# Kernel optimization log

Measured on AMD Instinct MI355X. Metric: run time of the kernel, lower is better.

Reference implementation:

```python
import jax, jax.numpy as jnp
import numpy as np

Q, N, FDIM, HDIM = 4096, 1024, 64, 128


def setup_inputs() -> dict:
    key = jax.random.key(0)
    ks = jax.random.split(key, 7)
    s = 0.05
    return {
        "query_points": jax.random.normal(ks[0], (Q, 3), dtype=jnp.float32),
        "node_features": jax.random.normal(ks[1], (N, FDIM), dtype=jnp.float32),
        "node_positions": jax.random.normal(ks[2], (N, 3), dtype=jnp.float32),
        # attention MLP: Linear(F+3 -> H), ReLU, Linear(H -> 1)
        "aW1": jax.random.normal(ks[3], (FDIM + 3, HDIM), dtype=jnp.float32) * s,
        "ab1": jnp.zeros((HDIM,), dtype=jnp.float32),
        "aW2": jax.random.normal(ks[4], (HDIM, 1), dtype=jnp.float32) * s,
        "ab2": jnp.zeros((1,), dtype=jnp.float32),
        # decoder MLP: Linear(F -> H), ReLU, Linear(H -> 3)
        "dW1": jax.random.normal(ks[5], (FDIM, HDIM), dtype=jnp.float32) * s,
        "db1": jnp.zeros((HDIM,), dtype=jnp.float32),
        "dW2": jax.random.normal(ks[6], (HDIM, 3), dtype=jnp.float32) * s,
        "db2": jnp.zeros((3,), dtype=jnp.float32),
    }


def reference(query_points, node_features, node_positions,
              aW1, ab1, aW2, ab2, dW1, db1, dW2, db2):
    F = node_features.shape[1]
    # pairwise offsets: [Q, N, 3]
    diff = query_points[:, None, :] - node_positions[None, :, :]
    # xy-plane distance -> inverse-distance weights: [Q, N, 1]
    dist = jnp.linalg.norm(diff[..., :2], axis=-1, keepdims=True)
    w = 1.0 / (dist + 1e-6)
    # attn MLP on concat([node_features, diff]); split W1 so the feature
    # part ([N,F]@[F,H]) is computed once instead of per query pair.
    h = jax.nn.relu(node_features @ aW1[:F] + diff @ aW1[F:] + ab1)  # [Q, N, H]
    score = h @ aW2 + ab2                                            # [Q, N, 1]
    attn = jax.nn.softmax(score * w, axis=1)                         # [Q, N, 1]
    agg = jnp.einsum('qn,nf->qf', attn[..., 0], node_features)       # [Q, F]
    return jax.nn.relu(agg @ dW1 + db1) @ dW2 + db2                  # [Q, 3]
```

## Files before the change

kernel.cpp:

```cpp
#include <hip/hip_runtime.h>
#include <math.h>

#define QN 4096
#define NN 1024
#define FD 64
#define HD 128

#define OFF_UT    0
#define OFF_B     524288
#define OFF_L     655360
#define OFF_PM    4849664
#define OFF_PART  4980736
#define OFF_SPART 7077888

__global__ __launch_bounds__(256) void k1_prep(
    const float* __restrict__ qp, const float* __restrict__ nf,
    const float* __restrict__ npos, const float* __restrict__ aW1,
    const float* __restrict__ ab1, float* __restrict__ B, float* __restrict__ UT) {
  int idx = blockIdx.x * 256 + threadIdx.x;
  if (idx < QN * HD) {
    int h = idx >> 12, q = idx & 4095;
    UT[idx] = qp[q*3+0] * aW1[(FD+0)*HD + h]
            + qp[q*3+1] * aW1[(FD+1)*HD + h]
            + qp[q*3+2] * aW1[(FD+2)*HD + h];
  } else {
    int i2 = idx - QN * HD;
    if (i2 < NN * HD) {
      int n = i2 >> 7, h = i2 & 127;
      float s = ab1[h];
      #pragma unroll
      for (int f = 0; f < FD; ++f) s = fmaf(nf[n*FD+f], aW1[f*HD+h], s);
      s -= npos[n*3+0] * aW1[(FD+0)*HD + h]
         + npos[n*3+1] * aW1[(FD+1)*HD + h]
         + npos[n*3+2] * aW1[(FD+2)*HD + h];
      B[i2] = s;
    }
  }
}

__global__ __launch_bounds__(256) void k2_logits(
    const float* __restrict__ Bg, const float* __restrict__ UT,
    const float* __restrict__ aW2, const float* __restrict__ ab2,
    const float* __restrict__ qp, const float* __restrict__ npos,
    float* __restrict__ L, float* __restrict__ pm) {
  __shared__ float Bs[32 * HD];
  __shared__ float red[4][4][64];
  const int q0 = blockIdx.x * 256, n0 = blockIdx.y * 32;
  const int t = threadIdx.x;
  {
    const float4* src = (const float4*)(Bg + n0 * HD);
    float4* dst = (float4*)Bs;
    #pragma unroll
    for (int r = 0; r < 4; ++r) dst[r*256 + t] = src[r*256 + t];
  }
  __syncthreads();
  const int lane = t & 63, w = t >> 6;
  const int nb = w * 8;

  float acc[4][8];
  #pragma unroll
  for (int qq = 0; qq < 4; ++qq)
    #pragma unroll
    for (int nn = 0; nn < 8; ++nn) acc[qq][nn] = 0.f;

  for (int hc = 0; hc < 16; ++hc) {
    float u[4][8];
    #pragma unroll
    for (int hh = 0; hh < 8; ++hh) {
      const float* up = UT + (hc*8 + hh) * QN + q0 + lane;
      #pragma unroll
      for (int qq = 0; qq < 4; ++qq) u[qq][hh] = up[qq*64];
    }
    float v[8];
    #pragma unroll
    for (int hh = 0; hh < 8; ++hh) v[hh] = aW2[hc*8 + hh];

    #pragma unroll
    for (int nn = 0; nn < 8; ++nn) {
      const float4* bp = (const float4*)(Bs + (nb + nn) * HD + hc*8);
      float4 b0 = bp[0], b1 = bp[1];
      float bb[8] = {b0.x, b0.y, b0.z, b0.w, b1.x, b1.y, b1.z, b1.w};
      #pragma unroll
      for (int qq = 0; qq < 4; ++qq) {
        #pragma unroll
        for (int hh = 0; hh < 8; ++hh) {
          float r = fmaxf(bb[hh] + u[qq][hh], 0.f);
          acc[qq][nn] = fmaf(r, v[hh], acc[qq][nn]);
        }
      }
    }
  }

  const float bias2 = ab2[0];
  float qx[4], qy[4], m4[4];
  #pragma unroll
  for (int qq = 0; qq < 4; ++qq) {
    int q = q0 + qq*64 + lane;
    qx[qq] = qp[q*3+0];
    qy[qq] = qp[q*3+1];
    m4[qq] = -3.4e38f;
  }
  #pragma unroll
  for (int nn = 0; nn < 8; ++nn) {
    int n = n0 + nb + nn;
    float px = npos[n*3+0], py = npos[n*3+1];
    #pragma unroll
    for (int qq = 0; qq < 4; ++qq) {
      float dx = qx[qq] - px, dy = qy[qq] - py;
      float wgt = 1.f / (sqrtf(dx*dx + dy*dy) + 1e-6f);
      float lg = (acc[qq][nn] + bias2) * wgt;
      L[n * QN + q0 + qq*64 + lane] = lg;
      m4[qq] = fmaxf(m4[qq], lg);
    }
  }
  #pragma unroll
  for (int qq = 0; qq < 4; ++qq) red[w][qq][lane] = m4[qq];
  __syncthreads();
  {
    int qq = t >> 6, ll = t & 63;
    float mm = fmaxf(fmaxf(red[0][qq][ll], red[1][qq][ll]),
                     fmaxf(red[2][qq][ll], red[3][qq][ll]));
    pm[(q0 + qq*64 + ll) * 32 + blockIdx.y] = mm;
  }
}

__global__ __launch_bounds__(256) void k4_agg(
    const float* __restrict__ L, const float* __restrict__ pm,
    const float* __restrict__ nf, float* __restrict__ part,
    float* __restrict__ spart) {
  __shared__ float red[4][32][64];
  __shared__ float sred[4][64];
  int b = blockIdx.x;
  int qt = b & 63, c = b >> 6;
  int t = threadIdx.x, lane = t & 63, w = t >> 6;
  int q = qt * 64 + lane;

  float m = -3.4e38f;
  {
    const float4* pmq = (const float4*)(pm + q * 32);
    #pragma unroll
    for (int g = 0; g < 8; ++g) {
      float4 pv = pmq[g];
      m = fmaxf(m, fmaxf(fmaxf(pv.x, pv.y), fmaxf(pv.z, pv.w)));
    }
  }

  float acc[64];
  #pragma unroll
  for (int f = 0; f < 64; ++f) acc[f] = 0.f;
  float s = 0.f;

  int nbase = c * 128 + w * 32;
  for (int i = 0; i < 32; ++i) {
    int n = nbase + i;
    float p = exp2f((L[n * QN + q] - m) * 1.44269504088896f);
    s += p;
    const float4* nfr = (const float4*)(nf + n * FD);
    #pragma unroll
    for (int g = 0; g < 4; ++g) {
      float4 a0 = nfr[g*4+0], a1 = nfr[g*4+1], a2 = nfr[g*4+2], a3 = nfr[g*4+3];
      acc[g*16+ 0] = fmaf(p, a0.x, acc[g*16+ 0]);
      acc[g*16+ 1] = fmaf(p, a0.y, acc[g*16+ 1]);
      acc[g*16+ 2] = fmaf(p, a0.z, acc[g*16+ 2]);
      acc[g*16+ 3] = fmaf(p, a0.w, acc[g*16+ 3]);
      acc[g*16+ 4] = fmaf(p, a1.x, acc[g*16+ 4]);
      acc[g*16+ 5] = fmaf(p, a1.y, acc[g*16+ 5]);
      acc[g*16+ 6] = fmaf(p, a1.z, acc[g*16+ 6]);
      acc[g*16+ 7] = fmaf(p, a1.w, acc[g*16+ 7]);
      acc[g*16+ 8] = fmaf(p, a2.x, acc[g*16+ 8]);
      acc[g*16+ 9] = fmaf(p, a2.y, acc[g*16+ 9]);
      acc[g*16+10] = fmaf(p, a2.z, acc[g*16+10]);
      acc[g*16+11] = fmaf(p, a2.w, acc[g*16+11]);
      acc[g*16+12] = fmaf(p, a3.x, acc[g*16+12]);
      acc[g*16+13] = fmaf(p, a3.y, acc[g*16+13]);
      acc[g*16+14] = fmaf(p, a3.z, acc[g*16+14]);
      acc[g*16+15] = fmaf(p, a3.w, acc[g*16+15]);
    }
  }

  sred[w][lane] = s;
  #pragma unroll
  for (int f = 0; f < 32; ++f) red[w][f][lane] = acc[f];
  __syncthreads();
  for (int idx = t; idx < 2048; idx += 256) {
    int f = idx >> 6, qq = idx & 63;
    float sum = red[0][f][qq] + red[1][f][qq] + red[2][f][qq] + red[3][f][qq];
    part[(c*64 + f) * QN + qt*64 + qq] = sum;
  }
  __syncthreads();
  #pragma unroll
  for (int f = 0; f < 32; ++f) red[w][f][lane] = acc[32 + f];
  __syncthreads();
  for (int idx = t; idx < 2048; idx += 256) {
    int f = idx >> 6, qq = idx & 63;
    float sum = red[0][f][qq] + red[1][f][qq] + red[2][f][qq] + red[3][f][qq];
    part[(c*64 + 32 + f) * QN + qt*64 + qq] = sum;
  }
  __syncthreads();
  if (t < 64) {
    spart[c * QN + qt*64 + t] = sred[0][t] + sred[1][t] + sred[2][t] + sred[3][t];
  }
}

__global__ __launch_bounds__(256) void k5_dec(
    const float* __restrict__ part, const float* __restrict__ spart,
    const float* __restrict__ dW1, const float* __restrict__ db1,
    const float* __restrict__ dW2, const float* __restrict__ db2,
    float* __restrict__ out) {
  __shared__ float aggL[2][64];
  __shared__ float h1s[2][128];
  int t = threadIdx.x;
  int qb = blockIdx.x * 2;
  if (t < 128) {
    int q2 = t >> 6, f = t & 63;
    int q = qb + q2;
    float v = 0.f;
    #pragma unroll
    for (int c = 0; c < 8; ++c) v += part[(c*64 + f) * QN + q];
    float s = 0.f;
    #pragma unroll
    for (int c = 0; c < 8; ++c) s += spart[c * QN + q];
    aggL[q2][f] = v / s;
  }
  __syncthreads();
  {
    int q2 = t >> 7, h = t & 127;
    float a = db1[h];
    #pragma unroll
    for (int f = 0; f < 64; ++f) a = fmaf(aggL[q2][f], dW1[f*HD + h], a);
    h1s[q2][h] = fmaxf(a, 0.f);
  }
  __syncthreads();
  if (t < 6) {
    int q2 = t / 3, o = t % 3;
    float a = db2[o];
    #pragma unroll
    for (int h = 0; h < 128; ++h) a = fmaf(h1s[q2][h], dW2[h*3 + o], a);
    out[(qb + q2) * 3 + o] = a;
  }
}

extern "C" void kernel_launch(void* const* d_in, const int* in_sizes, int n_in,
                              void* d_out, int out_size, void* d_ws, size_t ws_size,
                              hipStream_t stream) {
  const float* qp   = (const float*)d_in[0];
  const float* nf   = (const float*)d_in[1];
  const float* npos = (const float*)d_in[2];
  const float* aW1  = (const float*)d_in[3];
  const float* ab1  = (const float*)d_in[4];
  const float* aW2  = (const float*)d_in[5];
  const float* ab2  = (const float*)d_in[6];
  const float* dW1  = (const float*)d_in[7];
  const float* db1  = (const float*)d_in[8];
  const float* dW2  = (const float*)d_in[9];
  const float* db2  = (const float*)d_in[10];

  float* ws    = (float*)d_ws;
  float* UT    = ws + OFF_UT;
  float* B     = ws + OFF_B;
  float* L     = ws + OFF_L;
  float* pm    = ws + OFF_PM;
  float* part  = ws + OFF_PART;
  float* spart = ws + OFF_SPART;

  hipLaunchKernelGGL(k1_prep, dim3(2560), dim3(256), 0, stream,
                     qp, nf, npos, aW1, ab1, B, UT);
  hipLaunchKernelGGL(k2_logits, dim3(16, 32), dim3(256), 0, stream,
                     B, UT, aW2, ab2, qp, npos, L, pm);
  hipLaunchKernelGGL(k4_agg, dim3(512), dim3(256), 0, stream, L, pm, nf, part, spart);
  hipLaunchKernelGGL(k5_dec, dim3(2048), dim3(256), 0, stream,
                     part, spart, dW1, db1, dW2, db2, (float*)d_out);
}
```

Measured before the change: 121.9 us.

## Halve logits node tile, double-buffer U loads, transpose partials, batch decoder queries

The logits kernel now gives each block 16 nodes instead of 32, doubling the grid. It also loads the U tiles in a software-pipelined double buffer with an occupancy hint in launch bounds. The partial-aggregate layout becomes query-major so the decoder can read it coalesced, with the LDS reduction buffer padded. The decoder handles 16 queries per block and folds the softmax normalisation after the first matmul. The aim is better occupancy and latency hiding in the dominant kernel and fewer, more efficient decoder blocks, at the cost of more redundant U reads across node tiles.

```diff
diff --git a/kernel.cpp b/kernel.cpp
--- a/kernel.cpp
+++ b/kernel.cpp
@@ -10,8 +10,8 @@
 #define OFF_B     524288
 #define OFF_L     655360
 #define OFF_PM    4849664
-#define OFF_PART  4980736
-#define OFF_SPART 7077888
+#define OFF_PART  5111808
+#define OFF_SPART 7208960
 
 __global__ __launch_bounds__(256) void k1_prep(
     const float* __restrict__ qp, const float* __restrict__ nf,
@@ -38,58 +38,63 @@
   }
 }
 
-__global__ __launch_bounds__(256) void k2_logits(
+
+#define LOADU(dst, hcv) { \
+  const float* up_ = uptr + (hcv)*8*QN; \
+  _Pragma("unroll") for (int hh = 0; hh < 8; ++hh) \
+    _Pragma("unroll") for (int qq = 0; qq < 4; ++qq) \
+      dst[qq][hh] = up_[hh*QN + qq*64]; }
+
+#define COMPUTE(u, hcv) { \
+  float vv[8]; \
+  _Pragma("unroll") for (int hh = 0; hh < 8; ++hh) vv[hh] = aW2[(hcv)*8 + hh]; \
+  _Pragma("unroll") for (int nn = 0; nn < 4; ++nn) { \
+    const float4* bp = (const float4*)(Bs + (nb + nn) * HD + (hcv)*8); \
+    float4 b0 = bp[0], b1 = bp[1]; \
+    float bb[8] = {b0.x,b0.y,b0.z,b0.w,b1.x,b1.y,b1.z,b1.w}; \
+    _Pragma("unroll") for (int qq = 0; qq < 4; ++qq) \
+      _Pragma("unroll") for (int hh = 0; hh < 8; ++hh) { \
+        float r = fmaxf(bb[hh] + u[qq][hh], 0.f); \
+        acc[qq][nn] = fmaf(r, vv[hh], acc[qq][nn]); } } }
+
+__global__ __launch_bounds__(256, 4) void k2_logits(
     const float* __restrict__ Bg, const float* __restrict__ UT,
     const float* __restrict__ aW2, const float* __restrict__ ab2,
     const float* __restrict__ qp, const float* __restrict__ npos,
     float* __restrict__ L, float* __restrict__ pm) {
-  __shared__ float Bs[32 * HD];
+  __shared__ float Bs[16 * HD];
   __shared__ float red[4][4][64];
-  const int q0 = blockIdx.x * 256, n0 = blockIdx.y * 32;
+  const int q0 = blockIdx.x * 256, n0 = blockIdx.y * 16;
   const int t = threadIdx.x;
   {
     const float4* src = (const float4*)(Bg + n0 * HD);
     float4* dst = (float4*)Bs;
     #pragma unroll
-    for (int r = 0; r < 4; ++r) dst[r*256 + t] = src[r*256 + t];
+    for (int r = 0; r < 2; ++r) dst[r*256 + t] = src[r*256 + t];
   }
   __syncthreads();
   const int lane = t & 63, w = t >> 6;
-  const int nb = w * 8;
-
-  float acc[4][8];
+  const int nb = w * 4;
+  const float* uptr = UT + q0 + lane;
+
+  float acc[4][4];
   #pragma unroll
   for (int qq = 0; qq < 4; ++qq)
     #pragma unroll
-    for (int nn = 0; nn < 8; ++nn) acc[qq][nn] = 0.f;
-
-  for (int hc = 0; hc < 16; ++hc) {
-    float u[4][8];
-    #pragma unroll
-    for (int hh = 0; hh < 8; ++hh) {
-      const float* up = UT + (hc*8 + hh) * QN + q0 + lane;
-      #pragma unroll
-      for (int qq = 0; qq < 4; ++qq) u[qq][hh] = up[qq*64];
-    }
-    float v[8];
-    #pragma unroll
-    for (int hh = 0; hh < 8; ++hh) v[hh] = aW2[hc*8 + hh];
-
-    #pragma unroll
-    for (int nn = 0; nn < 8; ++nn) {
-      const float4* bp = (const float4*)(Bs + (nb + nn) * HD + hc*8);
-      float4 b0 = bp[0], b1 = bp[1];
-      float bb[8] = {b0.x, b0.y, b0.z, b0.w, b1.x, b1.y, b1.z, b1.w};
-      #pragma unroll
-      for (int qq = 0; qq < 4; ++qq) {
-        #pragma unroll
-        for (int hh = 0; hh < 8; ++hh) {
-          float r = fmaxf(bb[hh] + u[qq][hh], 0.f);
-          acc[qq][nn] = fmaf(r, v[hh], acc[qq][nn]);
-        }
-      }
-    }
-  }
+    for (int nn = 0; nn < 4; ++nn) acc[qq][nn] = 0.f;
+
+  float uA[4][8], uB[4][8];
+  LOADU(uA, 0);
+  #pragma unroll 1
+  for (int hc = 0; hc < 14; hc += 2) {
+    LOADU(uB, hc + 1);
+    COMPUTE(uA, hc);
+    LOADU(uA, hc + 2);
+    COMPUTE(uB, hc + 1);
+  }
+  LOADU(uB, 15);
+  COMPUTE(uA, 14);
+  COMPUTE(uB, 15);
 
   const float bias2 = ab2[0];
   float qx[4], qy[4], m4[4];
@@ -101,7 +106,7 @@
     m4[qq] = -3.4e38f;
   }
   #pragma unroll
-  for (int nn = 0; nn < 8; ++nn) {
+  for (int nn = 0; nn < 4; ++nn) {
     int n = n0 + nb + nn;
     float px = npos[n*3+0], py = npos[n*3+1];
     #pragma unroll
@@ -120,7 +125,7 @@
     int qq = t >> 6, ll = t & 63;
     float mm = fmaxf(fmaxf(red[0][qq][ll], red[1][qq][ll]),
                      fmaxf(red[2][qq][ll], red[3][qq][ll]));
-    pm[(q0 + qq*64 + ll) * 32 + blockIdx.y] = mm;
+    pm[(q0 + qq*64 + ll) * 64 + blockIdx.y] = mm;
   }
 }
 
@@ -128,7 +133,7 @@
     const float* __restrict__ L, const float* __restrict__ pm,
     const float* __restrict__ nf, float* __restrict__ part,
     float* __restrict__ spart) {
-  __shared__ float red[4][32][64];
+  __shared__ float red[4][32][65];
   __shared__ float sred[4][64];
   int b = blockIdx.x;
   int qt = b & 63, c = b >> 6;
@@ -137,9 +142,9 @@
 
   float m = -3.4e38f;
   {
-    const float4* pmq = (const float4*)(pm + q * 32);
-    #pragma unroll
-    for (int g = 0; g < 8; ++g) {
+    const float4* pmq = (const float4*)(pm + q * 64);
+    #pragma unroll
+    for (int g = 0; g < 16; ++g) {
       float4 pv = pmq[g];
       m = fmaxf(m, fmaxf(fmaxf(pv.x, pv.y), fmaxf(pv.z, pv.w)));
     }
@@ -183,18 +188,18 @@
   for (int f = 0; f < 32; ++f) red[w][f][lane] = acc[f];
   __syncthreads();
   for (int idx = t; idx < 2048; idx += 256) {
-    int f = idx >> 6, qq = idx & 63;
-    float sum = red[0][f][qq] + red[1][f][qq] + red[2][f][qq] + red[3][f][qq];
-    part[(c*64 + f) * QN + qt*64 + qq] = sum;
+    int qq = idx >> 5, fr = idx & 31;
+    float sum = red[0][fr][qq] + red[1][fr][qq] + red[2][fr][qq] + red[3][fr][qq];
+    part[(c * QN + qt*64 + qq) * 64 + fr] = sum;
   }
   __syncthreads();
   #pragma unroll
   for (int f = 0; f < 32; ++f) red[w][f][lane] = acc[32 + f];
   __syncthreads();
   for (int idx = t; idx < 2048; idx += 256) {
-    int f = idx >> 6, qq = idx & 63;
-    float sum = red[0][f][qq] + red[1][f][qq] + red[2][f][qq] + red[3][f][qq];
-    part[(c*64 + 32 + f) * QN + qt*64 + qq] = sum;
+    int qq = idx >> 5, fr = idx & 31;
+    float sum = red[0][fr][qq] + red[1][fr][qq] + red[2][fr][qq] + red[3][fr][qq];
+    part[(c * QN + qt*64 + qq) * 64 + 32 + fr] = sum;
   }
   __syncthreads();
   if (t < 64) {
@@ -207,36 +212,47 @@
     const float* __restrict__ dW1, const float* __restrict__ db1,
     const float* __restrict__ dW2, const float* __restrict__ db2,
     float* __restrict__ out) {
-  __shared__ float aggL[2][64];
-  __shared__ float h1s[2][128];
+  __shared__ float agg[16][64];
+  __shared__ float inv[16];
+  __shared__ float h1s[16][128];
   int t = threadIdx.x;
-  int qb = blockIdx.x * 2;
-  if (t < 128) {
-    int q2 = t >> 6, f = t & 63;
-    int q = qb + q2;
-    float v = 0.f;
-    #pragma unroll
-    for (int c = 0; c < 8; ++c) v += part[(c*64 + f) * QN + q];
+  int qb = blockIdx.x * 16;
+  if (t < 16) {
     float s = 0.f;
     #pragma unroll
-    for (int c = 0; c < 8; ++c) s += spart[c * QN + q];
-    aggL[q2][f] = v / s;
-  }
-  __syncthreads();
-  {
-    int q2 = t >> 7, h = t & 127;
-    float a = db1[h];
-    #pragma unroll
-    for (int f = 0; f < 64; ++f) a = fmaf(aggL[q2][f], dW1[f*HD + h], a);
-    h1s[q2][h] = fmaxf(a, 0.f);
-  }
-  __syncthreads();
-  if (t < 6) {
-    int q2 = t / 3, o = t % 3;
+    for (int c = 0; c < 8; ++c) s += spart[c*QN + qb + t];
+    inv[t] = 1.f / s;
+  }
+  {
+    int f = t & 63, qh = t >> 6;
+    #pragma unroll
+    for (int pass = 0; pass < 4; ++pass) {
+      int qs = pass*4 + qh;
+      float v = 0.f;
+      #pragma unroll
+      for (int c = 0; c < 8; ++c) v += part[(c*QN + qb + qs)*64 + f];
+      agg[qs][f] = v;
+    }
+  }
+  __syncthreads();
+  {
+    int h = t & 127, qg = t >> 7;
+    #pragma unroll
+    for (int k = 0; k < 8; ++k) {
+      int qs = qg*8 + k;
+      float a = 0.f;
+      #pragma unroll
+      for (int f = 0; f < 64; ++f) a = fmaf(agg[qs][f], dW1[f*HD + h], a);
+      h1s[qs][h] = fmaxf(a * inv[qs] + db1[h], 0.f);
+    }
+  }
+  __syncthreads();
+  if (t < 48) {
+    int qs = t / 3, o = t % 3;
     float a = db2[o];
     #pragma unroll
-    for (int h = 0; h < 128; ++h) a = fmaf(h1s[q2][h], dW2[h*3 + o], a);
-    out[(qb + q2) * 3 + o] = a;
+    for (int h = 0; h < HD; ++h) a = fmaf(h1s[qs][h], dW2[h*3 + o], a);
+    out[(qb + qs)*3 + o] = a;
   }
 }
 
@@ -265,9 +281,9 @@
 
   hipLaunchKernelGGL(k1_prep, dim3(2560), dim3(256), 0, stream,
                      qp, nf, npos, aW1, ab1, B, UT);
-  hipLaunchKernelGGL(k2_logits, dim3(16, 32), dim3(256), 0, stream,
+  hipLaunchKernelGGL(k2_logits, dim3(16, 64), dim3(256), 0, stream,
                      B, UT, aW2, ab2, qp, npos, L, pm);
   hipLaunchKernelGGL(k4_agg, dim3(512), dim3(256), 0, stream, L, pm, nf, part, spart);
-  hipLaunchKernelGGL(k5_dec, dim3(2048), dim3(256), 0, stream,
+  hipLaunchKernelGGL(k5_dec, dim3(256), dim3(256), 0, stream,
                      part, spart, dW1, db1, dW2, db2, (float*)d_out);
 }
```

Measured after the change: 336.5 us. 2.76x slower.
